# Performance work log

Measured on AMD Instinct MI355X. Metric: run time of the kernel, lower is better.

## Reference

```python
import jax, jax.numpy as jnp
import numpy as np

N, CAMS = 1, 4
C1, C2, NH = 256, 256, 8
H1, H2, W2 = 128, 64, 400
H, W = 128, 128


def setup_inputs() -> dict:
    key = jax.random.key(0)
    ks = jax.random.split(key, 16)
    sc = 0.02
    th = jax.random.uniform(ks[3], (N, CAMS)) * 2.0 * np.pi
    c, s = jnp.cos(th), jnp.sin(th)
    z, o = jnp.zeros_like(c), jnp.ones_like(c)
    rots = jnp.stack([jnp.stack([c, -s, z], -1), jnp.stack([s, c, z], -1), jnp.stack([z, z, o], -1)], -2)
    return {
        "list_a": jax.random.normal(ks[0], (N, C1, H, W), jnp.float32),
        "list_b": jax.random.normal(ks[1], (N * CAMS, C2, H2, W2), jnp.float32),
        "fov_list": jax.random.uniform(ks[2], (N, CAMS)) * 0.5 + 1.0,
        "rots_list": rots.astype(jnp.float32),
        "trans_list": jax.random.normal(ks[4], (N, CAMS, 3), jnp.float32),
        "fxs": jax.random.uniform(ks[5], (N, CAMS)) * 100.0 + 500.0,
        "cxs": jax.random.uniform(ks[6], (N, CAMS)) * 20.0 + 390.0,
        "pos_a": jax.random.normal(ks[7], (1, H1, C1), jnp.float32),
        "pos_b": jax.random.normal(ks[8], (1, H2, C2), jnp.float32),
        "Wq": jax.random.normal(ks[9], (C1, C1), jnp.float32) * sc,
        "bq": jnp.zeros((C1,), jnp.float32),
        "Wk": jax.random.normal(ks[10], (C1, C2), jnp.float32) * sc,
        "bk": jnp.zeros((C1,), jnp.float32),
        "Wv": jax.random.normal(ks[11], (C1, C2), jnp.float32) * sc,
        "bv": jnp.zeros((C1,), jnp.float32),
        "in_w": jax.random.normal(ks[12], (3 * C1, C1), jnp.float32) * sc,
        "in_b": jnp.zeros((3 * C1,), jnp.float32),
        "out_w": jax.random.normal(ks[13], (C1, C1), jnp.float32) * sc,
        "out_b": jnp.zeros((C1,), jnp.float32),
    }


def _polar_coords(w1, h1, Hh, Ww, rots, fx, cx):
    # per-pixel viewing angles from intrinsics (original image width hard-coded 800)
    pi = jnp.arange(w1, dtype=jnp.float32)
    pw = 800.0 / w1
    ang = jnp.arctan((pi * pw + pw / 2.0 - cx) / fx)
    R90 = jnp.array([[0.0, 1.0], [-1.0, 0.0]], jnp.float32)
    rot = R90 @ rots[:2, :2].astype(jnp.float32)
    cr, sr = rot[0, 0], rot[1, 0]
    ca = cr * jnp.cos(ang) + sr * jnp.sin(ang)
    sa = -sr * jnp.cos(ang) + cr * jnp.sin(ang)
    cxp = jnp.float32(Ww // 2)
    cyp = jnp.float32(Hh // 2)
    rmax = jnp.sqrt(cxp ** 2 + cyp ** 2)
    radii = jnp.linspace(0.0, 1.0, h1).reshape(h1, 1) * rmax
    x = cxp + radii * ca  # [h1, w1]
    y = cyp - radii * sa
    return x, y


def _bilinear(img, x, y):
    # img [C,H,W]; x,y pixel coords [h1,w1]; grid_sample(align_corners=True) after clamping
    Hh, Ww = img.shape[1], img.shape[2]
    x = jnp.clip(x, 0.0, Ww - 1.0)
    y = jnp.clip(y, 0.0, Hh - 1.0)
    x0 = jnp.floor(x); y0 = jnp.floor(y)
    x1 = jnp.clip(x0 + 1.0, 0.0, Ww - 1.0)
    y1 = jnp.clip(y0 + 1.0, 0.0, Hh - 1.0)
    wx = x - x0; wy = y - y0
    x0i, x1i = x0.astype(jnp.int32), x1.astype(jnp.int32)
    y0i, y1i = y0.astype(jnp.int32), y1.astype(jnp.int32)
    v00 = img[:, y0i, x0i]; v01 = img[:, y0i, x1i]
    v10 = img[:, y1i, x0i]; v11 = img[:, y1i, x1i]
    return v00 * (1 - wx) * (1 - wy) + v01 * wx * (1 - wy) + v10 * (1 - wx) * wy + v11 * wx * wy


def _mha(q, k, v, in_w, in_b, out_w, out_b, nh):
    E = q.shape[-1]
    dh = E // nh
    qq = q @ in_w[:E].T + in_b[:E]
    kk = k @ in_w[E:2 * E].T + in_b[E:2 * E]
    vv = v @ in_w[2 * E:].T + in_b[2 * E:]
    B, Lq, _ = q.shape
    Lk = k.shape[1]
    qq = qq.reshape(B, Lq, nh, dh)
    kk = kk.reshape(B, Lk, nh, dh)
    vv = vv.reshape(B, Lk, nh, dh)
    att = jnp.einsum('bqhd,bkhd->bhqk', qq, kk) / jnp.sqrt(jnp.float32(dh))
    p = jax.nn.softmax(att, axis=-1)
    o = jnp.einsum('bhqk,bkhd->bqhd', p, vv).reshape(B, Lq, E)
    return o @ out_w.T + out_b


def _forward(list_a, list_b, rots_list, fxs, cxs, pos_a, pos_b,
             Wq, bq, Wk, bk, Wv, bv, in_w, in_b, out_w, out_b):
    outs = []
    for i in range(list_a.shape[0]):
        a = list_a[i]
        C1_, h1, Wb = a.shape
        Hb = h1
        enh = None
        for j in (0, 3):  # cameras 1 and 2 are skipped by the original `continue`
            b = list_b[i * CAMS + j]
            C2_, h2, w2 = b.shape
            x, y = _polar_coords(w2, h1, a.shape[1], a.shape[2], rots_list[i, j], fxs[i, j], cxs[i, j])
            a_rect = _bilinear(a, x, y)                     # [C1, h1, w2]
            a_seq = jnp.transpose(a_rect, (2, 1, 0)) + pos_a  # [w2, h1, C1]
            b_seq = jnp.transpose(b, (2, 1, 0)) + pos_b       # [w2, h2, C2]
            q = a_seq @ Wq.T + bq
            k = b_seq @ Wk.T + bk
            v = b_seq @ Wv.T + bv
            o = _mha(q, k, v, in_w, in_b, out_w, out_b, NH)
            a_enh = jnp.transpose(o, (2, 1, 0))              # [C1, h1, w2]
            # scatter-add restore with nearest-pixel indices
            xi = jnp.clip(jnp.round(x), 0, a.shape[2] - 1).astype(jnp.int32)
            yi = jnp.clip(jnp.round(y), 0, a.shape[1] - 1).astype(jnp.int32)
            idx = (yi * a.shape[2] + xi).reshape(-1)
            vals = a_enh.reshape(C1_, -1)
            rest = jnp.zeros((C1_, a.shape[1] * a.shape[2]), a.dtype).at[:, idx].add(vals)
            cnt = jnp.zeros((a.shape[1] * a.shape[2],), a.dtype).at[idx].add(1.0)
            cnt = jnp.where(cnt == 0, 1.0, cnt)
            enh = (rest / cnt).reshape(a.shape)
            a = a + enh
        outs.append(a + enh)  # original double-adds the last camera's enhancement
    return jnp.stack(outs)


def reference(list_a, list_b, fov_list, rots_list, trans_list, fxs, cxs, pos_a, pos_b,
              Wq, bq, Wk, bk, Wv, bv, in_w, in_b, out_w, out_b):
    # fov_list / trans_list are accepted but unused in the original math path
    return _forward(list_a, list_b, rots_list, fxs, cxs, pos_a, pos_b,
                    Wq, bq, Wk, bk, Wv, bv, in_w, in_b, out_w, out_b)
```

## Files before the change

### kernel.cpp

```cpp
#include <hip/hip_runtime.h>

#define PIX 16384
#define MS 51200
#define MB 25600

typedef __attribute__((ext_vector_type(8))) short short8;
typedef __attribute__((ext_vector_type(4))) float floatx4;

__device__ inline ushort f2b(float x) {
  uint u = __float_as_uint(x);
  return (ushort)((u + 0x7fffu + ((u >> 16) & 1u)) >> 16);
}
__device__ inline float b2f(ushort u) {
  return __uint_as_float(((uint)u) << 16);
}

__global__ __launch_bounds__(256) void coords_kernel(
    const float* __restrict__ rots, const float* __restrict__ fxs,
    const float* __restrict__ cxs, int j,
    float* __restrict__ xarr, float* __restrict__ yarr,
    int* __restrict__ idxarr, float* __restrict__ cnt)
{
  int s = blockIdx.x * 256 + threadIdx.x;
  int h = s / 400;
  int w = s - h * 400;
  float fx = fxs[j], cx = cxs[j];
  const float* R = rots + j * 9;
  float cr = R[3];
  float sr = -R[0];
  float t = (2.0f * (float)w + 1.0f - cx) / fx;
  float inv = 1.0f / sqrtf(1.0f + t * t);
  float ca = (cr + sr * t) * inv;
  float sa = (cr * t - sr) * inv;
  float rad = ((float)h * (1.0f / 127.0f)) * 90.50966799187808f;
  float x = 64.0f + rad * ca;
  float y = 64.0f - rad * sa;
  xarr[s] = x;
  yarr[s] = y;
  int xi = (int)fminf(fmaxf(rintf(x), 0.0f), 127.0f);
  int yi = (int)fminf(fmaxf(rintf(y), 0.0f), 127.0f);
  int pix = yi * 128 + xi;
  idxarr[s] = pix;
  atomicAdd(&cnt[pix], 1.0f);
}

__global__ __launch_bounds__(256) void prefix_kernel(
    const float* __restrict__ cnt, int* __restrict__ offsets)
{
  __shared__ int sh[256];
  int t = threadIdx.x;
  int base = t * 64;
  const float4* cp = (const float4*)(cnt + base);
  int sum = 0;
#pragma unroll
  for (int i = 0; i < 16; ++i) {
    float4 v = cp[i];
    sum += (int)v.x + (int)v.y + (int)v.z + (int)v.w;
  }
  sh[t] = sum;
  __syncthreads();
  for (int d = 1; d < 256; d <<= 1) {
    int v = (t >= d) ? sh[t - d] : 0;
    __syncthreads();
    sh[t] += v;
    __syncthreads();
  }
  int run = sh[t] - sum;
  int4* op = (int4*)(offsets + base);
#pragma unroll
  for (int i = 0; i < 16; ++i) {
    float4 v = cp[i];
    int a0 = (int)v.x, a1 = (int)v.y, a2 = (int)v.z, a3 = (int)v.w;
    int4 o;
    o.x = run; o.y = run + a0; o.z = run + a0 + a1; o.w = run + a0 + a1 + a2;
    op[i] = o;
    run += a0 + a1 + a2 + a3;
  }
}

__global__ __launch_bounds__(256) void fill_kernel(
    const int* __restrict__ idxarr, const int* __restrict__ offsets,
    int* __restrict__ cursor, int* __restrict__ order, int* __restrict__ pixs)
{
  int s = blockIdx.x * 256 + threadIdx.x;
  int pix = idxarr[s];
  int pos = offsets[pix] + atomicAdd(&cursor[pix], 1);
  order[pos] = (s % 400) * 128 + (s / 400);
  pixs[pos] = pix;
}

__global__ __launch_bounds__(256) void transpose_kernel(
    const float* __restrict__ src, ushort* __restrict__ dst, int W)
{
  __shared__ float tile[64][65];
  int p0 = blockIdx.x * 64;
  int c0 = blockIdx.y * 64;
  int t = threadIdx.x;
  int pr = (t & 15) * 4;
  int cr = t >> 4;
#pragma unroll
  for (int q = 0; q < 4; ++q) {
    int c = cr + q * 16;
    float4 v = *(const float4*)(src + (size_t)(c0 + c) * W + p0 + pr);
    tile[pr + 0][c] = v.x;
    tile[pr + 1][c] = v.y;
    tile[pr + 2][c] = v.z;
    tile[pr + 3][c] = v.w;
  }
  __syncthreads();
  int p = t >> 2;
  int ch = (t & 3) * 16;
  ushort tmp[16];
#pragma unroll
  for (int i = 0; i < 16; ++i) tmp[i] = f2b(tile[p][ch + i]);
  ushort* d = dst + (size_t)(p0 + p) * 256 + c0 + ch;
  *(uint4*)(d) = *(uint4*)tmp;
  *(uint4*)(d + 8) = *(uint4*)(tmp + 8);
}

__global__ __launch_bounds__(256) void f2b_kernel(
    const float* __restrict__ in, ushort* __restrict__ out)
{
  int t = blockIdx.x * 256 + threadIdx.x;
  float4 v = ((const float4*)in)[t];
  ushort4 o;
  o.x = f2b(v.x); o.y = f2b(v.y); o.z = f2b(v.z); o.w = f2b(v.w);
  ((ushort4*)out)[t] = o;
}

#define LFP 264
__global__ __launch_bounds__(256) void sampleproj_kernel(
    const ushort* __restrict__ aT, const float* __restrict__ xarr,
    const float* __restrict__ yarr, const ushort* __restrict__ Wh,
    const float* __restrict__ bias, ushort* __restrict__ qh)
{
  __shared__ ushort lf[64 * LFP];
  int s0 = blockIdx.x * 64;
  int tid = threadIdx.x;
  int lane = tid & 63;
  int wave = tid >> 6;
  int col = lane & 15, quad = lane >> 4;
  int c0 = lane * 4;

#pragma unroll 4
  for (int i = 0; i < 16; ++i) {
    int sl = wave * 16 + i;
    int s = s0 + sl;
    float x = fminf(fmaxf(xarr[s], 0.0f), 127.0f);
    float y = fminf(fmaxf(yarr[s], 0.0f), 127.0f);
    float x0f = floorf(x), y0f = floorf(y);
    int x0 = (int)x0f, y0 = (int)y0f;
    int x1 = min(x0 + 1, 127), y1 = min(y0 + 1, 127);
    float wx = x - x0f, wy = y - y0f;
    float w00 = (1.0f - wx) * (1.0f - wy);
    float w01 = wx * (1.0f - wy);
    float w10 = (1.0f - wx) * wy;
    float w11 = wx * wy;
    ushort4 v00 = *(const ushort4*)(aT + (size_t)(y0 * 128 + x0) * 256 + c0);
    ushort4 v01 = *(const ushort4*)(aT + (size_t)(y0 * 128 + x1) * 256 + c0);
    ushort4 v10 = *(const ushort4*)(aT + (size_t)(y1 * 128 + x0) * 256 + c0);
    ushort4 v11 = *(const ushort4*)(aT + (size_t)(y1 * 128 + x1) * 256 + c0);
    ushort4 o;
    o.x = f2b(w00 * b2f(v00.x) + w01 * b2f(v01.x) + w10 * b2f(v10.x) + w11 * b2f(v11.x));
    o.y = f2b(w00 * b2f(v00.y) + w01 * b2f(v01.y) + w10 * b2f(v10.y) + w11 * b2f(v11.y));
    o.z = f2b(w00 * b2f(v00.z) + w01 * b2f(v01.z) + w10 * b2f(v10.z) + w11 * b2f(v11.z));
    o.w = f2b(w00 * b2f(v00.w) + w01 * b2f(v01.w) + w10 * b2f(v10.w) + w11 * b2f(v11.w));
    *(ushort4*)&lf[sl * LFP + c0] = o;
  }
  __syncthreads();

  int fw = wave * 64;
  floatx4 acc[4][4];
#pragma unroll
  for (int i = 0; i < 4; ++i)
#pragma unroll
    for (int jx = 0; jx < 4; ++jx) acc[i][jx] = (floatx4){0.f, 0.f, 0.f, 0.f};

  for (int kb = 0; kb < 256; kb += 32) {
    short8 aop[4], bop[4];
#pragma unroll
    for (int tf = 0; tf < 4; ++tf)
      aop[tf] = *(const short8*)(Wh + (size_t)(fw + tf * 16 + col) * 256 + kb + quad * 8);
#pragma unroll
    for (int ts = 0; ts < 4; ++ts)
      bop[ts] = *(const short8*)&lf[(ts * 16 + col) * LFP + kb + quad * 8];
#pragma unroll
    for (int ts = 0; ts < 4; ++ts)
#pragma unroll
      for (int tf = 0; tf < 4; ++tf)
        acc[ts][tf] = __builtin_amdgcn_mfma_f32_16x16x32_bf16(
            aop[tf], bop[ts], acc[ts][tf], 0, 0, 0);
  }
#pragma unroll
  for (int ts = 0; ts < 4; ++ts) {
    int s = s0 + ts * 16 + col;
    int h = s / 400;
    int w = s - h * 400;
    size_t obase = (size_t)(w * 128 + h) * 256;
#pragma unroll
    for (int tf = 0; tf < 4; ++tf) {
      int f = fw + tf * 16 + quad * 4;
      float4 bv = *(const float4*)(bias + h * 256 + f);
      ushort4 ov;
      ov.x = f2b(acc[ts][tf][0] + bv.x);
      ov.y = f2b(acc[ts][tf][1] + bv.y);
      ov.z = f2b(acc[ts][tf][2] + bv.z);
      ov.w = f2b(acc[ts][tf][3] + bv.w);
      *(ushort4*)(qh + obase + f) = ov;
    }
  }
}

__global__ __launch_bounds__(256) void projKV_kernel(
    const ushort* __restrict__ featB,
    const ushort* __restrict__ WhK, const ushort* __restrict__ WhV,
    const float* __restrict__ biasK, const float* __restrict__ biasV,
    ushort* __restrict__ kh, ushort* __restrict__ vh)
{
  int m0 = blockIdx.x * 64;
  int lane = threadIdx.x & 63;
  int wave = threadIdx.x >> 6;
  int col = lane & 15, quad = lane >> 4;
  int fw = wave * 64;

  floatx4 accK[4][4], accV[4][4];
#pragma unroll
  for (int i = 0; i < 4; ++i)
#pragma unroll
    for (int jx = 0; jx < 4; ++jx) {
      accK[i][jx] = (floatx4){0.f, 0.f, 0.f, 0.f};
      accV[i][jx] = (floatx4){0.f, 0.f, 0.f, 0.f};
    }

  for (int kb = 0; kb < 256; kb += 32) {
    short8 bop[4];
#pragma unroll
    for (int ts = 0; ts < 4; ++ts)
      bop[ts] = *(const short8*)(featB + (size_t)(m0 + ts * 16 + col) * 256 + kb + quad * 8);
    short8 aK[4];
#pragma unroll
    for (int tf = 0; tf < 4; ++tf)
      aK[tf] = *(const short8*)(WhK + (size_t)(fw + tf * 16 + col) * 256 + kb + quad * 8);
#pragma unroll
    for (int ts = 0; ts < 4; ++ts)
#pragma unroll
      for (int tf = 0; tf < 4; ++tf)
        accK[ts][tf] = __builtin_amdgcn_mfma_f32_16x16x32_bf16(
            aK[tf], bop[ts], accK[ts][tf], 0, 0, 0);
    short8 aV[4];
#pragma unroll
    for (int tf = 0; tf < 4; ++tf)
      aV[tf] = *(const short8*)(WhV + (size_t)(fw + tf * 16 + col) * 256 + kb + quad * 8);
#pragma unroll
    for (int ts = 0; ts < 4; ++ts)
#pragma unroll
      for (int tf = 0; tf < 4; ++tf)
        accV[ts][tf] = __builtin_amdgcn_mfma_f32_16x16x32_bf16(
            aV[tf], bop[ts], accV[ts][tf], 0, 0, 0);
  }
#pragma unroll
  for (int ts = 0; ts < 4; ++ts) {
    int m = m0 + ts * 16 + col;
    int h = m / 400;
    int w = m - h * 400;
    size_t obase = (size_t)(w * 64 + h) * 256;
#pragma unroll
    for (int tf = 0; tf < 4; ++tf) {
      int f = fw + tf * 16 + quad * 4;
      float4 bvK = *(const float4*)(biasK + h * 256 + f);
      ushort4 ovK;
      ovK.x = f2b(accK[ts][tf][0] + bvK.x);
      ovK.y = f2b(accK[ts][tf][1] + bvK.y);
      ovK.z = f2b(accK[ts][tf][2] + bvK.z);
      ovK.w = f2b(accK[ts][tf][3] + bvK.w);
      *(ushort4*)(kh + obase + f) = ovK;
      float4 bvV = *(const float4*)(biasV + h * 256 + f);
      ushort4 ovV;
      ovV.x = f2b(accV[ts][tf][0] + bvV.x);
      ovV.y = f2b(accV[ts][tf][1] + bvV.y);
      ovV.z = f2b(accV[ts][tf][2] + bvV.z);
      ovV.w = f2b(accV[ts][tf][3] + bvV.w);
      *(ushort4*)(vh + obase + f) = ovV;
    }
  }
}

#define VP 72
#define PP 72
__global__ __launch_bounds__(256) void attn_mfma_kernel(
    const ushort* __restrict__ qh, const ushort* __restrict__ kh,
    const ushort* __restrict__ vh, ushort* __restrict__ obuf)
{
  __shared__ ushort lV[4][32 * VP];
  __shared__ ushort lP[4][16 * PP];
  int b = blockIdx.x;
  int wave = threadIdx.x >> 6;
  int lane = threadIdx.x & 63;
  int head = blockIdx.y * 4 + wave;
  int col = lane & 15, quad = lane >> 4;
  ushort* Vw = lV[wave];
  ushort* Pw = lP[wave];

  short8 bk0 = *(const short8*)(kh + ((size_t)(b * 64 +  0 + col)) * 256 + head * 32 + quad * 8);
  short8 bk1 = *(const short8*)(kh + ((size_t)(b * 64 + 16 + col)) * 256 + head * 32 + quad * 8);
  short8 bk2 = *(const short8*)(kh + ((size_t)(b * 64 + 32 + col)) * 256 + head * 32 + quad * 8);
  short8 bk3 = *(const short8*)(kh + ((size_t)(b * 64 + 48 + col)) * 256 + head * 32 + quad * 8);

  {
    const ushort* vsrc = vh + ((size_t)(b * 64 + lane)) * 256 + head * 32;
    ushort vr[32];
    *(uint4*)(vr) = *(const uint4*)(vsrc);
    *(uint4*)(vr + 8) = *(const uint4*)(vsrc + 8);
    *(uint4*)(vr + 16) = *(const uint4*)(vsrc + 16);
    *(uint4*)(vr + 24) = *(const uint4*)(vsrc + 24);
#pragma unroll
    for (int d = 0; d < 32; ++d) Vw[d * VP + lane] = vr[d];
  }
  short8 vA0 = *(const short8*)(Vw + (col) * VP + 0 * 32 + quad * 8);
  short8 vB0 = *(const short8*)(Vw + (16 + col) * VP + 0 * 32 + quad * 8);
  short8 vA1 = *(const short8*)(Vw + (col) * VP + 1 * 32 + quad * 8);
  short8 vB1 = *(const short8*)(Vw + (16 + col) * VP + 1 * 32 + quad * 8);

  const float scl = 0.17677669529663687f;
  for (int qt = 0; qt < 8; ++qt) {
    short8 aq = *(const short8*)(qh +
        ((size_t)(b * 128 + qt * 16 + col)) * 256 + head * 32 + quad * 8);
    floatx4 s0 = {0.f,0.f,0.f,0.f}, s1 = s0, s2 = s0, s3 = s0;
    s0 = __builtin_amdgcn_mfma_f32_16x16x32_bf16(aq, bk0, s0, 0, 0, 0);
    s1 = __builtin_amdgcn_mfma_f32_16x16x32_bf16(aq, bk1, s1, 0, 0, 0);
    s2 = __builtin_amdgcn_mfma_f32_16x16x32_bf16(aq, bk2, s2, 0, 0, 0);
    s3 = __builtin_amdgcn_mfma_f32_16x16x32_bf16(aq, bk3, s3, 0, 0, 0);
    float e[4][4], mr[4], sm[4];
#pragma unroll
    for (int r = 0; r < 4; ++r) {
      float v0 = s0[r] * scl, v1 = s1[r] * scl;
      float v2 = s2[r] * scl, v3 = s3[r] * scl;
      e[0][r] = v0; e[1][r] = v1; e[2][r] = v2; e[3][r] = v3;
      mr[r] = fmaxf(fmaxf(v0, v1), fmaxf(v2, v3));
    }
#pragma unroll
    for (int mask = 1; mask <= 8; mask <<= 1)
#pragma unroll
      for (int r = 0; r < 4; ++r)
        mr[r] = fmaxf(mr[r], __shfl_xor(mr[r], mask, 64));
#pragma unroll
    for (int r = 0; r < 4; ++r) {
      float acc = 0.f;
#pragma unroll
      for (int t = 0; t < 4; ++t) {
        float ev = __expf(e[t][r] - mr[r]);
        e[t][r] = ev;
        acc += ev;
      }
      sm[r] = acc;
    }
#pragma unroll
    for (int mask = 1; mask <= 8; mask <<= 1)
#pragma unroll
      for (int r = 0; r < 4; ++r)
        sm[r] += __shfl_xor(sm[r], mask, 64);
#pragma unroll
    for (int t = 0; t < 4; ++t)
#pragma unroll
      for (int r = 0; r < 4; ++r)
        Pw[(quad * 4 + r) * PP + t * 16 + col] = f2b(e[t][r]);
    floatx4 o0 = {0.f,0.f,0.f,0.f}, o1 = o0;
    {
      short8 ap0 = *(const short8*)(Pw + col * PP + 0 * 32 + quad * 8);
      o0 = __builtin_amdgcn_mfma_f32_16x16x32_bf16(ap0, vA0, o0, 0, 0, 0);
      o1 = __builtin_amdgcn_mfma_f32_16x16x32_bf16(ap0, vB0, o1, 0, 0, 0);
      short8 ap1 = *(const short8*)(Pw + col * PP + 1 * 32 + quad * 8);
      o0 = __builtin_amdgcn_mfma_f32_16x16x32_bf16(ap1, vA1, o0, 0, 0, 0);
      o1 = __builtin_amdgcn_mfma_f32_16x16x32_bf16(ap1, vB1, o1, 0, 0, 0);
    }
#pragma unroll
    for (int r = 0; r < 4; ++r) {
      float iv = 1.0f / sm[r];
      size_t row = (size_t)(b * 128 + qt * 16 + quad * 4 + r) * 256 + head * 32;
      obuf[row + col] = f2b(o0[r] * iv);
      obuf[row + 16 + col] = f2b(o1[r] * iv);
    }
  }
}

__global__ __launch_bounds__(256) void gemmN_kernel(
    const float* __restrict__ A, const float* __restrict__ Wt,
    const float* __restrict__ biasf, float* __restrict__ Cout, int mode)
{
  __shared__ float As[64][17];
  __shared__ float Ws[16][65];
  int m0 = blockIdx.x * 64;
  int n0 = blockIdx.y * 64;
  int tid = threadIdx.x;
  int tx = tid & 15, ty = tid >> 4;
  float acc[4][4] = {};
  for (int k0 = 0; k0 < 256; k0 += 16) {
    {
      int m = tid >> 2;
      int kq = (tid & 3) << 2;
      float4 v = *(const float4*)(A + (size_t)(m0 + m) * 256 + k0 + kq);
      As[m][kq + 0] = v.x; As[m][kq + 1] = v.y;
      As[m][kq + 2] = v.z; As[m][kq + 3] = v.w;
    }
    {
      int f = tid >> 2;
      int kq = (tid & 3) << 2;
      float4 v = *(const float4*)(Wt + (size_t)(n0 + f) * 256 + k0 + kq);
      Ws[kq + 0][f] = v.x; Ws[kq + 1][f] = v.y;
      Ws[kq + 2][f] = v.z; Ws[kq + 3][f] = v.w;
    }
    __syncthreads();
#pragma unroll
    for (int kk = 0; kk < 16; ++kk) {
      float a[4], b[4];
#pragma unroll
      for (int i = 0; i < 4; ++i) a[i] = As[ty * 4 + i][kk];
#pragma unroll
      for (int jj = 0; jj < 4; ++jj) b[jj] = Ws[kk][tx * 4 + jj];
#pragma unroll
      for (int i = 0; i < 4; ++i)
#pragma unroll
        for (int jj = 0; jj < 4; ++jj) acc[i][jj] += a[i] * b[jj];
    }
    __syncthreads();
  }
#pragma unroll
  for (int i = 0; i < 4; ++i) {
    int m = m0 + ty * 4 + i;
    int f = n0 + tx * 4;
    float4 ov;
    if (mode == 0) {
      float4 bv = *(const float4*)(biasf + f);
      ov.x = acc[i][0] + bv.x; ov.y = acc[i][1] + bv.y;
      ov.z = acc[i][2] + bv.z; ov.w = acc[i][3] + bv.w;
    } else {
      ov.x = acc[i][0]; ov.y = acc[i][1];
      ov.z = acc[i][2]; ov.w = acc[i][3];
    }
    *(float4*)(Cout + (size_t)m * 256 + f) = ov;
  }
}

__global__ __launch_bounds__(256) void gemm_ab_kernel(
    const float* __restrict__ in_w, const float* __restrict__ Wq,
    const float* __restrict__ Wk, const float* __restrict__ Wv,
    float* __restrict__ weff, ushort* __restrict__ weffh)
{
  int z = blockIdx.z;
  const float* A = in_w + (size_t)z * 65536;
  const float* B = (z == 0) ? Wq : ((z == 1) ? Wk : Wv);
  float* C = weff + (size_t)z * 65536;
  ushort* Ch = weffh + (size_t)z * 65536;
  __shared__ float As[64][17];
  __shared__ float Bs[16][64];
  int m0 = blockIdx.x * 64;
  int n0 = blockIdx.y * 64;
  int tid = threadIdx.x;
  int tx = tid & 15, ty = tid >> 4;
  float acc[4][4] = {};
  for (int k0 = 0; k0 < 256; k0 += 16) {
    {
      int m = tid >> 2;
      int kq = (tid & 3) << 2;
      float4 v = *(const float4*)(A + (size_t)(m0 + m) * 256 + k0 + kq);
      As[m][kq + 0] = v.x; As[m][kq + 1] = v.y;
      As[m][kq + 2] = v.z; As[m][kq + 3] = v.w;
    }
    {
      int k = tid >> 4;
      int nq = (tid & 15) << 2;
      float4 v = *(const float4*)(B + (size_t)(k0 + k) * 256 + n0 + nq);
      *(float4*)(&Bs[k][nq]) = v;
    }
    __syncthreads();
#pragma unroll
    for (int kk = 0; kk < 16; ++kk) {
      float a[4], b[4];
#pragma unroll
      for (int i = 0; i < 4; ++i) a[i] = As[ty * 4 + i][kk];
#pragma unroll
      for (int jj = 0; jj < 4; ++jj) b[jj] = Bs[kk][tx * 4 + jj];
#pragma unroll
      for (int i = 0; i < 4; ++i)
#pragma unroll
        for (int jj = 0; jj < 4; ++jj) acc[i][jj] += a[i] * b[jj];
    }
    __syncthreads();
  }
#pragma unroll
  for (int i = 0; i < 4; ++i) {
    int m = m0 + ty * 4 + i;
    *(float4*)(C + (size_t)m * 256 + n0 + tx * 4) = *(float4*)&acc[i][0];
    ushort4 hv;
    hv.x = f2b(acc[i][0]); hv.y = f2b(acc[i][1]);
    hv.z = f2b(acc[i][2]); hv.w = f2b(acc[i][3]);
    *(ushort4*)(Ch + (size_t)m * 256 + n0 + tx * 4) = hv;
  }
}

__global__ void beff_kernel(const float* __restrict__ in_w, const float* __restrict__ in_b,
                            const float* __restrict__ bq, const float* __restrict__ bk,
                            const float* __restrict__ bv, float* __restrict__ beff)
{
  int z = blockIdx.x;
  int f = threadIdx.x;
  const float* bsrc = (z == 0) ? bq : ((z == 1) ? bk : bv);
  const float* row = in_w + (size_t)(z * 256 + f) * 256;
  float acc = in_b[z * 256 + f];
  for (int e = 0; e < 256; ++e) acc += row[e] * bsrc[e];
  beff[z * 256 + f] = acc;
}

#define CH 64
__global__ __launch_bounds__(256) void segred_kernel(
    const ushort* __restrict__ obuf, const int* __restrict__ order,
    const int* __restrict__ pixs, float* __restrict__ osum)
{
  __shared__ int lm[CH];
  __shared__ int lp[CH + 2];
  int s0 = blockIdx.x * CH;
  int t = threadIdx.x;
  if (t < CH) {
    lm[t] = order[s0 + t];
    lp[t + 1] = pixs[s0 + t];
  } else if (t == CH) {
    lp[0] = (s0 > 0) ? pixs[s0 - 1] : -1;
  } else if (t == CH + 1) {
    lp[CH + 1] = (s0 + CH < MS) ? pixs[s0 + CH] : -2;
  }
  __syncthreads();
  int c = t;
  float va[8];
#pragma unroll
  for (int k = 0; k < 8; ++k)
    va[k] = b2f(obuf[(size_t)lm[k] * 256 + c]);
  float acc = 0.0f;
  int runBegin = 0;
#pragma unroll
  for (int i = 0; i < CH; ++i) {
    float v = va[i & 7];
    if (i + 8 < CH) va[i & 7] = b2f(obuf[(size_t)lm[i + 8] * 256 + c]);
    acc += v;
    int p = lp[i + 1];
    bool last = (i == CH - 1);
    if (last || p != lp[i + 2]) {
      bool pBeg = (runBegin == 0) && (p == lp[0]);
      bool pEnd = last && (p == lp[CH + 1]);
      float* dst = osum + (size_t)p * 256 + c;
      if (pBeg || pEnd) atomicAdd(dst, acc);
      else *dst = acc;
      acc = 0.0f;
      runBegin = i + 1;
    }
  }
}

__global__ __launch_bounds__(256) void outproj_update_kernel(
    const float* __restrict__ osum, const ushort* __restrict__ out_wh,
    const float* __restrict__ asrc, float* __restrict__ adst,
    const float* __restrict__ cnt, const float* __restrict__ out_b,
    float scale)
{
  int p0 = blockIdx.x * 64;
  int lane = threadIdx.x & 63;
  int wave = threadIdx.x >> 6;
  int col = lane & 15, quad = lane >> 4;
  int fw = wave * 64;
  floatx4 acc[4][4];
#pragma unroll
  for (int i = 0; i < 4; ++i)
#pragma unroll
    for (int jx = 0; jx < 4; ++jx) acc[i][jx] = (floatx4){0.f, 0.f, 0.f, 0.f};

  for (int kb = 0; kb < 256; kb += 32) {
    short8 aop[4], bop[4];
#pragma unroll
    for (int tf = 0; tf < 4; ++tf)
      aop[tf] = *(const short8*)(out_wh +
          (size_t)(fw + tf * 16 + col) * 256 + kb + quad * 8);
#pragma unroll
    for (int ts = 0; ts < 4; ++ts) {
      const float* brow = osum + (size_t)(p0 + ts * 16 + col) * 256 + kb + quad * 8;
      float4 f0 = *(const float4*)brow;
      float4 f1 = *(const float4*)(brow + 4);
      short8 bv;
      bv[0] = (short)f2b(f0.x); bv[1] = (short)f2b(f0.y);
      bv[2] = (short)f2b(f0.z); bv[3] = (short)f2b(f0.w);
      bv[4] = (short)f2b(f1.x); bv[5] = (short)f2b(f1.y);
      bv[6] = (short)f2b(f1.z); bv[7] = (short)f2b(f1.w);
      bop[ts] = bv;
    }
#pragma unroll
    for (int ts = 0; ts < 4; ++ts)
#pragma unroll
      for (int tf = 0; tf < 4; ++tf)
        acc[ts][tf] = __builtin_amdgcn_mfma_f32_16x16x32_bf16(
            aop[tf], bop[ts], acc[ts][tf], 0, 0, 0);
  }
#pragma unroll
  for (int ts = 0; ts < 4; ++ts) {
    int p = p0 + ts * 16 + col;
    float cn = cnt[p];
    float rs = scale / fmaxf(cn, 1.0f);
#pragma unroll
    for (int tf = 0; tf < 4; ++tf) {
      int f = fw + tf * 16 + quad * 4;
      float4 ob = *(const float4*)(out_b + f);
      adst[(size_t)(f + 0) * PIX + p] = asrc[(size_t)(f + 0) * PIX + p] + (acc[ts][tf][0] + cn * ob.x) * rs;
      adst[(size_t)(f + 1) * PIX + p] = asrc[(size_t)(f + 1) * PIX + p] + (acc[ts][tf][1] + cn * ob.y) * rs;
      adst[(size_t)(f + 2) * PIX + p] = asrc[(size_t)(f + 2) * PIX + p] + (acc[ts][tf][2] + cn * ob.z) * rs;
      adst[(size_t)(f + 3) * PIX + p] = asrc[(size_t)(f + 3) * PIX + p] + (acc[ts][tf][3] + cn * ob.w) * rs;
    }
  }
}

extern "C" void kernel_launch(void* const* d_in, const int* in_sizes, int n_in,
                              void* d_out, int out_size, void* d_ws, size_t ws_size,
                              hipStream_t stream) {
  const float* list_a = (const float*)d_in[0];
  const float* list_b = (const float*)d_in[1];
  const float* rots   = (const float*)d_in[3];
  const float* fxs    = (const float*)d_in[5];
  const float* cxs    = (const float*)d_in[6];
  const float* pos_a  = (const float*)d_in[7];
  const float* pos_b  = (const float*)d_in[8];
  const float* Wq     = (const float*)d_in[9];
  const float* bq     = (const float*)d_in[10];
  const float* Wk     = (const float*)d_in[11];
  const float* bk     = (const float*)d_in[12];
  const float* Wv     = (const float*)d_in[13];
  const float* bv     = (const float*)d_in[14];
  const float* in_w   = (const float*)d_in[15];
  const float* in_b   = (const float*)d_in[16];
  const float* out_w  = (const float*)d_in[17];
  const float* out_b  = (const float*)d_in[18];

  float* ws      = (float*)d_ws;
  float* weff    = ws;
  float* beff    = weff + 196608;
  float* qpos    = beff + 768;
  float* kpos    = qpos + 32768;
  float* vpos    = kpos + 16384;
  float* a_cur   = vpos + 16384;
  float* xarr    = a_cur + 4194304;
  float* yarr    = xarr + 51200;
  int*   idxarr  = (int*)(yarr + 51200);
  float* cnt     = (float*)(idxarr + 51200);
  int*   cursor  = (int*)(cnt + 16384);
  int*   offs    = cursor + 16384;
  int*   order   = offs + 16384;
  int*   pixs    = order + 51200;
  float* osum    = (float*)(pixs + 51200);
  ushort* weffh  = (ushort*)(osum + 4194304);
  ushort* out_wh = weffh + 196608;
  ushort* obufh  = out_wh + 65536;
  ushort* bhT    = obufh + 13107200;
  ushort* qh     = bhT + 6553600;
  ushort* kh     = qh + 13107200;
  ushort* vh     = kh + 6553600;
  ushort* aT     = vh + 6553600;

  gemm_ab_kernel<<<dim3(4, 4, 3), 256, 0, stream>>>(in_w, Wq, Wk, Wv, weff, weffh);
  beff_kernel<<<3, 256, 0, stream>>>(in_w, in_b, bq, bk, bv, beff);
  f2b_kernel<<<64, 256, 0, stream>>>(out_w, out_wh);

  gemmN_kernel<<<dim3(2, 4), 256, 0, stream>>>(pos_a, weff, beff, qpos, 0);
  gemmN_kernel<<<dim3(1, 4), 256, 0, stream>>>(pos_b, weff + 65536, beff + 256, kpos, 0);
  gemmN_kernel<<<dim3(1, 4), 256, 0, stream>>>(pos_b, weff + 131072, beff + 512, vpos, 0);

  for (int jj = 0; jj < 2; ++jj) {
    int j = jj ? 3 : 0;
    const float* asrc = jj ? a_cur : list_a;
    hipMemsetAsync(cnt, 0, (size_t)2 * 16384 * sizeof(float), stream);
    hipMemsetAsync(osum, 0, (size_t)4194304 * sizeof(float), stream);
    coords_kernel<<<200, 256, 0, stream>>>(rots, fxs, cxs, j, xarr, yarr, idxarr, cnt);
    prefix_kernel<<<1, 256, 0, stream>>>(cnt, offs);
    fill_kernel<<<200, 256, 0, stream>>>(idxarr, offs, cursor, order, pixs);
    transpose_kernel<<<dim3(256, 4), 256, 0, stream>>>(asrc, aT, PIX);
    const float* bsrc = list_b + (size_t)j * 6553600;
    transpose_kernel<<<dim3(400, 4), 256, 0, stream>>>(bsrc, bhT, MB);
    sampleproj_kernel<<<800, 256, 0, stream>>>(aT, xarr, yarr, weffh, qpos, qh);
    projKV_kernel<<<400, 256, 0, stream>>>(bhT, weffh + 65536, weffh + 131072,
                                           kpos, vpos, kh, vh);
    attn_mfma_kernel<<<dim3(400, 2), 256, 0, stream>>>(qh, kh, vh, obufh);
    segred_kernel<<<800, 256, 0, stream>>>(obufh, order, pixs, osum);
    outproj_update_kernel<<<256, 256, 0, stream>>>(osum, out_wh, asrc,
                                                   jj ? (float*)d_out : a_cur,
                                                   cnt, out_b, jj ? 2.0f : 1.0f);
  }
}
```

Before: 676.9 us.

## Fuse feature transposes into consumers and batch coordinate setup across cameras

```diff
diff --git a/kernel.cpp b/kernel.cpp
--- a/kernel.cpp
+++ b/kernel.cpp
@@ -17,10 +17,12 @@
 
 __global__ __launch_bounds__(256) void coords_kernel(
     const float* __restrict__ rots, const float* __restrict__ fxs,
-    const float* __restrict__ cxs, int j,
+    const float* __restrict__ cxs,
     float* __restrict__ xarr, float* __restrict__ yarr,
     int* __restrict__ idxarr, float* __restrict__ cnt)
 {
+  int jz = blockIdx.y;
+  int j = jz ? 3 : 0;
   int s = blockIdx.x * 256 + threadIdx.x;
   int h = s / 400;
   int w = s - h * 400;
@@ -35,18 +37,20 @@
   float rad = ((float)h * (1.0f / 127.0f)) * 90.50966799187808f;
   float x = 64.0f + rad * ca;
   float y = 64.0f - rad * sa;
-  xarr[s] = x;
-  yarr[s] = y;
+  xarr[jz * MS + s] = x;
+  yarr[jz * MS + s] = y;
   int xi = (int)fminf(fmaxf(rintf(x), 0.0f), 127.0f);
   int yi = (int)fminf(fmaxf(rintf(y), 0.0f), 127.0f);
   int pix = yi * 128 + xi;
-  idxarr[s] = pix;
-  atomicAdd(&cnt[pix], 1.0f);
+  idxarr[jz * MS + s] = pix;
+  atomicAdd(&cnt[jz * PIX + pix], 1.0f);
 }
 
 __global__ __launch_bounds__(256) void prefix_kernel(
-    const float* __restrict__ cnt, int* __restrict__ offsets)
-{
+    const float* __restrict__ cntg, int* __restrict__ offsetsg)
+{
+  const float* cnt = cntg + blockIdx.x * PIX;
+  int* offsets = offsetsg + blockIdx.x * PIX;
   __shared__ int sh[256];
   int t = threadIdx.x;
   int base = t * 64;
@@ -82,15 +86,16 @@
     const int* __restrict__ idxarr, const int* __restrict__ offsets,
     int* __restrict__ cursor, int* __restrict__ order, int* __restrict__ pixs)
 {
+  int jz = blockIdx.y;
   int s = blockIdx.x * 256 + threadIdx.x;
-  int pix = idxarr[s];
-  int pos = offsets[pix] + atomicAdd(&cursor[pix], 1);
-  order[pos] = (s % 400) * 128 + (s / 400);
-  pixs[pos] = pix;
+  int pix = idxarr[jz * MS + s];
+  int pos = offsets[jz * PIX + pix] + atomicAdd(&cursor[jz * PIX + pix], 1);
+  order[jz * MS + pos] = (s % 400) * 128 + (s / 400);
+  pixs[jz * MS + pos] = pix;
 }
 
 __global__ __launch_bounds__(256) void transpose_kernel(
-    const float* __restrict__ src, ushort* __restrict__ dst, int W)
+    const float* __restrict__ src, ushort* __restrict__ dst)
 {
   __shared__ float tile[64][65];
   int p0 = blockIdx.x * 64;
@@ -101,7 +106,7 @@
 #pragma unroll
   for (int q = 0; q < 4; ++q) {
     int c = cr + q * 16;
-    float4 v = *(const float4*)(src + (size_t)(c0 + c) * W + p0 + pr);
+    float4 v = *(const float4*)(src + (size_t)(c0 + c) * PIX + p0 + pr);
     tile[pr + 0][c] = v.x;
     tile[pr + 1][c] = v.y;
     tile[pr + 2][c] = v.z;
@@ -211,17 +216,33 @@
   }
 }
 
+#define LBP 264
 __global__ __launch_bounds__(256) void projKV_kernel(
-    const ushort* __restrict__ featB,
+    const float* __restrict__ bsrc,
     const ushort* __restrict__ WhK, const ushort* __restrict__ WhV,
     const float* __restrict__ biasK, const float* __restrict__ biasV,
     ushort* __restrict__ kh, ushort* __restrict__ vh)
 {
+  __shared__ ushort lb[64 * LBP];
   int m0 = blockIdx.x * 64;
-  int lane = threadIdx.x & 63;
-  int wave = threadIdx.x >> 6;
+  int tid = threadIdx.x;
+  int lane = tid & 63;
+  int wave = tid >> 6;
   int col = lane & 15, quad = lane >> 4;
   int fw = wave * 64;
+
+  int pr = (tid & 15) * 4;
+  int cb = tid >> 4;
+#pragma unroll 4
+  for (int q = 0; q < 16; ++q) {
+    int c = cb + q * 16;
+    float4 v = *(const float4*)(bsrc + (size_t)c * MB + m0 + pr);
+    lb[(pr + 0) * LBP + c] = f2b(v.x);
+    lb[(pr + 1) * LBP + c] = f2b(v.y);
+    lb[(pr + 2) * LBP + c] = f2b(v.z);
+    lb[(pr + 3) * LBP + c] = f2b(v.w);
+  }
+  __syncthreads();
 
   floatx4 accK[4][4], accV[4][4];
 #pragma unroll
@@ -236,7 +257,7 @@
     short8 bop[4];
 #pragma unroll
     for (int ts = 0; ts < 4; ++ts)
-      bop[ts] = *(const short8*)(featB + (size_t)(m0 + ts * 16 + col) * 256 + kb + quad * 8);
+      bop[ts] = *(const short8*)&lb[(ts * 16 + col) * LBP + kb + quad * 8];
     short8 aK[4];
 #pragma unroll
     for (int tf = 0; tf < 4; ++tf)
@@ -383,10 +404,17 @@
   }
 }
 
-__global__ __launch_bounds__(256) void gemmN_kernel(
-    const float* __restrict__ A, const float* __restrict__ Wt,
-    const float* __restrict__ biasf, float* __restrict__ Cout, int mode)
-{
+__global__ __launch_bounds__(256) void gemmN3_kernel(
+    const float* __restrict__ pos_a, const float* __restrict__ pos_b,
+    const float* __restrict__ weff, const float* __restrict__ beff,
+    float* __restrict__ qpos, float* __restrict__ kpos, float* __restrict__ vpos)
+{
+  int z = blockIdx.z;
+  if (z > 0 && blockIdx.x > 0) return;
+  const float* A = (z == 0) ? pos_a : pos_b;
+  const float* Wt = weff + (size_t)z * 65536;
+  const float* biasf = beff + z * 256;
+  float* Cout = (z == 0) ? qpos : ((z == 1) ? kpos : vpos);
   __shared__ float As[64][17];
   __shared__ float Ws[16][65];
   int m0 = blockIdx.x * 64;
@@ -428,15 +456,10 @@
   for (int i = 0; i < 4; ++i) {
     int m = m0 + ty * 4 + i;
     int f = n0 + tx * 4;
+    float4 bv = *(const float4*)(biasf + f);
     float4 ov;
-    if (mode == 0) {
-      float4 bv = *(const float4*)(biasf + f);
-      ov.x = acc[i][0] + bv.x; ov.y = acc[i][1] + bv.y;
-      ov.z = acc[i][2] + bv.z; ov.w = acc[i][3] + bv.w;
-    } else {
-      ov.x = acc[i][0]; ov.y = acc[i][1];
-      ov.z = acc[i][2]; ov.w = acc[i][3];
-    }
+    ov.x = acc[i][0] + bv.x; ov.y = acc[i][1] + bv.y;
+    ov.z = acc[i][2] + bv.z; ov.w = acc[i][3] + bv.w;
     *(float4*)(Cout + (size_t)m * 256 + f) = ov;
   }
 }
@@ -559,7 +582,7 @@
     const float* __restrict__ osum, const ushort* __restrict__ out_wh,
     const float* __restrict__ asrc, float* __restrict__ adst,
     const float* __restrict__ cnt, const float* __restrict__ out_b,
-    float scale)
+    float scale, ushort* __restrict__ aTout, int writeAT)
 {
   int p0 = blockIdx.x * 64;
   int lane = threadIdx.x & 63;
@@ -606,10 +629,19 @@
     for (int tf = 0; tf < 4; ++tf) {
       int f = fw + tf * 16 + quad * 4;
       float4 ob = *(const float4*)(out_b + f);
-      adst[(size_t)(f + 0) * PIX + p] = asrc[(size_t)(f + 0) * PIX + p] + (acc[ts][tf][0] + cn * ob.x) * rs;
-      adst[(size_t)(f + 1) * PIX + p] = asrc[(size_t)(f + 1) * PIX + p] + (acc[ts][tf][1] + cn * ob.y) * rs;
-      adst[(size_t)(f + 2) * PIX + p] = asrc[(size_t)(f + 2) * PIX + p] + (acc[ts][tf][2] + cn * ob.z) * rs;
-      adst[(size_t)(f + 3) * PIX + p] = asrc[(size_t)(f + 3) * PIX + p] + (acc[ts][tf][3] + cn * ob.w) * rs;
+      float r0 = asrc[(size_t)(f + 0) * PIX + p] + (acc[ts][tf][0] + cn * ob.x) * rs;
+      float r1 = asrc[(size_t)(f + 1) * PIX + p] + (acc[ts][tf][1] + cn * ob.y) * rs;
+      float r2 = asrc[(size_t)(f + 2) * PIX + p] + (acc[ts][tf][2] + cn * ob.z) * rs;
+      float r3 = asrc[(size_t)(f + 3) * PIX + p] + (acc[ts][tf][3] + cn * ob.w) * rs;
+      adst[(size_t)(f + 0) * PIX + p] = r0;
+      adst[(size_t)(f + 1) * PIX + p] = r1;
+      adst[(size_t)(f + 2) * PIX + p] = r2;
+      adst[(size_t)(f + 3) * PIX + p] = r3;
+      if (writeAT) {
+        ushort4 hv;
+        hv.x = f2b(r0); hv.y = f2b(r1); hv.z = f2b(r2); hv.w = f2b(r3);
+        *(ushort4*)(aTout + (size_t)p * 256 + f) = hv;
+      }
     }
   }
 }
@@ -643,19 +675,18 @@
   float* vpos    = kpos + 16384;
   float* a_cur   = vpos + 16384;
   float* xarr    = a_cur + 4194304;
-  float* yarr    = xarr + 51200;
-  int*   idxarr  = (int*)(yarr + 51200);
-  float* cnt     = (float*)(idxarr + 51200);
-  int*   cursor  = (int*)(cnt + 16384);
-  int*   offs    = cursor + 16384;
-  int*   order   = offs + 16384;
-  int*   pixs    = order + 51200;
-  float* osum    = (float*)(pixs + 51200);
+  float* yarr    = xarr + 102400;
+  int*   idxarr  = (int*)(yarr + 102400);
+  int*   offs    = idxarr + 102400;
+  int*   order   = offs + 32768;
+  int*   pixs    = order + 102400;
+  float* cnt     = (float*)(pixs + 102400);
+  int*   cursor  = (int*)(cnt + 32768);
+  float* osum    = (float*)(cursor + 32768);
   ushort* weffh  = (ushort*)(osum + 4194304);
   ushort* out_wh = weffh + 196608;
   ushort* obufh  = out_wh + 65536;
-  ushort* bhT    = obufh + 13107200;
-  ushort* qh     = bhT + 6553600;
+  ushort* qh     = obufh + 13107200;
   ushort* kh     = qh + 13107200;
   ushort* vh     = kh + 6553600;
   ushort* aT     = vh + 6553600;
@@ -663,29 +694,30 @@
   gemm_ab_kernel<<<dim3(4, 4, 3), 256, 0, stream>>>(in_w, Wq, Wk, Wv, weff, weffh);
   beff_kernel<<<3, 256, 0, stream>>>(in_w, in_b, bq, bk, bv, beff);
   f2b_kernel<<<64, 256, 0, stream>>>(out_w, out_wh);
-
-  gemmN_kernel<<<dim3(2, 4), 256, 0, stream>>>(pos_a, weff, beff, qpos, 0);
-  gemmN_kernel<<<dim3(1, 4), 256, 0, stream>>>(pos_b, weff + 65536, beff + 256, kpos, 0);
-  gemmN_kernel<<<dim3(1, 4), 256, 0, stream>>>(pos_b, weff + 131072, beff + 512, vpos, 0);
+  gemmN3_kernel<<<dim3(2, 4, 3), 256, 0, stream>>>(pos_a, pos_b, weff, beff,
+                                                   qpos, kpos, vpos);
+  hipMemsetAsync(cnt, 0, (size_t)(32768 + 32768) * sizeof(float), stream);
+  coords_kernel<<<dim3(200, 2), 256, 0, stream>>>(rots, fxs, cxs, xarr, yarr, idxarr, cnt);
+  prefix_kernel<<<2, 256, 0, stream>>>(cnt, offs);
+  fill_kernel<<<dim3(200, 2), 256, 0, stream>>>(idxarr, offs, cursor, order, pixs);
 
   for (int jj = 0; jj < 2; ++jj) {
     int j = jj ? 3 : 0;
     const float* asrc = jj ? a_cur : list_a;
-    hipMemsetAsync(cnt, 0, (size_t)2 * 16384 * sizeof(float), stream);
     hipMemsetAsync(osum, 0, (size_t)4194304 * sizeof(float), stream);
-    coords_kernel<<<200, 256, 0, stream>>>(rots, fxs, cxs, j, xarr, yarr, idxarr, cnt);
-    prefix_kernel<<<1, 256, 0, stream>>>(cnt, offs);
-    fill_kernel<<<200, 256, 0, stream>>>(idxarr, offs, cursor, order, pixs);
-    transpose_kernel<<<dim3(256, 4), 256, 0, stream>>>(asrc, aT, PIX);
-    const float* bsrc = list_b + (size_t)j * 6553600;
-    transpose_kernel<<<dim3(400, 4), 256, 0, stream>>>(bsrc, bhT, MB);
-    sampleproj_kernel<<<800, 256, 0, stream>>>(aT, xarr, yarr, weffh, qpos, qh);
-    projKV_kernel<<<400, 256, 0, stream>>>(bhT, weffh + 65536, weffh + 131072,
+    if (jj == 0)
+      transpose_kernel<<<dim3(256, 4), 256, 0, stream>>>(list_a, aT);
+    sampleproj_kernel<<<800, 256, 0, stream>>>(aT, xarr + jj * MS, yarr + jj * MS,
+                                               weffh, qpos, qh);
+    projKV_kernel<<<400, 256, 0, stream>>>(list_b + (size_t)j * 6553600,
+                                           weffh + 65536, weffh + 131072,
                                            kpos, vpos, kh, vh);
     attn_mfma_kernel<<<dim3(400, 2), 256, 0, stream>>>(qh, kh, vh, obufh);
-    segred_kernel<<<800, 256, 0, stream>>>(obufh, order, pixs, osum);
+    segred_kernel<<<800, 256, 0, stream>>>(obufh, order + jj * MS, pixs + jj * MS, osum);
     outproj_update_kernel<<<256, 256, 0, stream>>>(osum, out_wh, asrc,
                                                    jj ? (float*)d_out : a_cur,
-                                                   cnt, out_b, jj ? 2.0f : 1.0f);
-  }
-}
+                                                   cnt + jj * PIX, out_b,
+                                                   jj ? 2.0f : 1.0f,
+                                                   aT, jj == 0 ? 1 : 0);
+  }
+}
```

After: 560.7 us. -17.2%, faster.
